# Optimization experiments

Hardware: AMD Instinct MI355X
Metric: run time of the kernel (lower is better)

The kernel has to match this reference:

```python
import jax, jax.numpy as jnp
import numpy as np

NEG_INF = -9e15
LEAKY_SLOPE = 0.01  # torch F.leaky_relu default


def setup_inputs() -> dict:
    key = jax.random.key(0)
    k1, k2, k3, k4 = jax.random.split(key, 4)
    N, F = 8192, 128
    inp = jax.random.normal(k1, (N, F), dtype=jnp.float32)
    adj = jax.random.randint(k2, (N, N), 0, 2, dtype=jnp.int32)
    # xavier_uniform with gain=1.414
    gain = 1.414
    limW = gain * np.sqrt(6.0 / (F + F))
    W = jax.random.uniform(k3, (F, F), minval=-limW, maxval=limW, dtype=jnp.float32)
    lima = gain * np.sqrt(6.0 / (2 * F + 1))
    a = jax.random.uniform(k4, (2 * F, 1), minval=-lima, maxval=lima, dtype=jnp.float32)
    return {"input": inp, "adj": adj, "W": W, "a": a}


def reference(input, adj, W, a):
    F_ = W.shape[0]
    h = input @ W                               # [N, F]
    # a_input[i,j] = concat(h[i], h[j]); (a_input @ a)[i,j] = h[i]@a1 + h[j]@a2
    a1, a2 = a[:F_, 0], a[F_:, 0]               # [F], [F]
    s1 = h @ a1                                 # [N]
    s2 = h @ a2                                 # [N]
    e = jax.nn.leaky_relu(s1[:, None] + s2[None, :], negative_slope=LEAKY_SLOPE)  # [N, N]
    masked = jnp.where(adj > 0, e, jnp.float32(NEG_INF))
    attention = jax.nn.softmax(masked, axis=1)  # [N, N]
    return attention @ h                        # [N, F]
```

## Files before the change

kernel.cpp:

```cpp
#include <hip/hip_runtime.h>
#include <hip/hip_bf16.h>

#define NN 8192
#define FF 128

typedef unsigned short ushort_t;
typedef __attribute__((ext_vector_type(4))) float f32x4;
typedef __attribute__((ext_vector_type(4))) int i32x4;
typedef __attribute__((ext_vector_type(8))) short s16x8;

__global__ __launch_bounds__(256)
void k1_hw(const float* __restrict__ inp, const float* __restrict__ W,
           const float* __restrict__ a, ushort_t* __restrict__ hT,
           float* __restrict__ s1g, float* __restrict__ Ug, float* __restrict__ Vg)
{
  __shared__ float Wl[FF * FF];
  __shared__ float il[32 * 129];
  __shared__ float red1[32 * 8];
  __shared__ float red2[32 * 8];
  const int t = threadIdx.x;
  const int ib = blockIdx.x * 32;

  {
    const float4* Ws = (const float4*)W;
    float4* Wd = (float4*)Wl;
#pragma unroll
    for (int q = 0; q < 16; ++q) Wd[t + 256 * q] = Ws[t + 256 * q];
  }
#pragma unroll
  for (int q = 0; q < 4; ++q) {
    int idx = t + 256 * q;
    int r = idx >> 5, c4 = idx & 31;
    float4 v = ((const float4*)(inp + (size_t)(ib + r) * FF))[c4];
    float* dst = &il[r * 129 + c4 * 4];
    dst[0] = v.x; dst[1] = v.y; dst[2] = v.z; dst[3] = v.w;
  }
  __syncthreads();

  const int r = t & 31;
  const int c0 = (t >> 5) * 16;
  float acc[16];
#pragma unroll
  for (int j = 0; j < 16; ++j) acc[j] = 0.f;

#pragma unroll 4
  for (int k = 0; k < FF; ++k) {
    float iv = il[r * 129 + k];
    const float4* wrow = (const float4*)&Wl[k * FF + c0];
    float4 w0 = wrow[0], w1 = wrow[1], w2 = wrow[2], w3 = wrow[3];
    acc[0]  += iv * w0.x; acc[1]  += iv * w0.y; acc[2]  += iv * w0.z; acc[3]  += iv * w0.w;
    acc[4]  += iv * w1.x; acc[5]  += iv * w1.y; acc[6]  += iv * w1.z; acc[7]  += iv * w1.w;
    acc[8]  += iv * w2.x; acc[9]  += iv * w2.y; acc[10] += iv * w2.z; acc[11] += iv * w2.w;
    acc[12] += iv * w3.x; acc[13] += iv * w3.y; acc[14] += iv * w3.z; acc[15] += iv * w3.w;
  }

  float ps1 = 0.f, ps2 = 0.f;
#pragma unroll
  for (int q = 0; q < 4; ++q) {
    float4 a1v = *(const float4*)(a + c0 + 4 * q);
    float4 a2v = *(const float4*)(a + FF + c0 + 4 * q);
    ps1 += acc[4*q+0]*a1v.x + acc[4*q+1]*a1v.y + acc[4*q+2]*a1v.z + acc[4*q+3]*a1v.w;
    ps2 += acc[4*q+0]*a2v.x + acc[4*q+1]*a2v.y + acc[4*q+2]*a2v.z + acc[4*q+3]*a2v.w;
  }
  red1[r * 8 + (t >> 5)] = ps1;
  red2[r * 8 + (t >> 5)] = ps2;

#pragma unroll
  for (int j = 0; j < 16; ++j) {
    unsigned b = __float_as_uint(acc[j]);
    hT[(unsigned)(c0 + j) * NN + (unsigned)(ib + r)] = (ushort_t)((b + 0x8000u) >> 16);
  }
  __syncthreads();
  if (t < 32) {
    float s1 = 0.f, s2 = 0.f;
#pragma unroll
    for (int g2 = 0; g2 < 8; ++g2) { s1 += red1[t * 8 + g2]; s2 += red2[t * 8 + g2]; }
    s1g[ib + t] = s1;
    Ug[ib + t] = expf(s2);
    Vg[ib + t] = expf(0.01f * s2);
  }
}

__global__ __launch_bounds__(512, 2)
void k3_attn(const int* __restrict__ adj, const float* __restrict__ s1g,
             const float* __restrict__ Ug, const float* __restrict__ Vg,
             const ushort_t* __restrict__ hT, float* __restrict__ out)
{
  __shared__ float accL[8][16][128];
  __shared__ float zL[8][16];

  const int t = threadIdx.x;
  const int lane = t & 63, w = t >> 6;
  const int rowl = lane & 15, kq = lane >> 4;
  const int rb = blockIdx.x * 16;
  const int jb = w * 1024 + kq * 8;

  const float s1v = s1g[rb + rowl];
  const float lv = s1v > 0.f ? s1v : 0.01f * s1v;
  const float P = expf(s1v - lv - 24.f);
  const float Q = expf(0.01f * s1v - lv - 24.f);
  const float E = expf(-s1v);

  f32x4 acc[8];
#pragma unroll
  for (int n = 0; n < 8; ++n) { acc[n][0] = 0.f; acc[n][1] = 0.f; acc[n][2] = 0.f; acc[n][3] = 0.f; }
  float z = 0.f;

  const i32x4* adjv = (const i32x4*)(adj + (size_t)(rb + rowl) * NN + jb);
  const float4* Uv = (const float4*)(Ug + jb);
  const float4* Vv = (const float4*)(Vg + jb);
  const ushort_t* hp[8];
#pragma unroll
  for (int n = 0; n < 8; ++n) hp[n] = hT + (size_t)(n * 16 + rowl) * NN + jb;

#pragma unroll 2
  for (int ks = 0; ks < 32; ++ks) {
    i32x4 A0 = __builtin_nontemporal_load(adjv + ks * 8);
    i32x4 A1 = __builtin_nontemporal_load(adjv + ks * 8 + 1);
    float4 u0 = Uv[ks * 8], u1 = Uv[ks * 8 + 1];
    float4 v0 = Vv[ks * 8], v1 = Vv[ks * 8 + 1];

    float w0 = u0.x > E ? P * u0.x : Q * v0.x;  w0 = A0[0] > 0 ? w0 : 0.f;
    float w1 = u0.y > E ? P * u0.y : Q * v0.y;  w1 = A0[1] > 0 ? w1 : 0.f;
    float w2 = u0.z > E ? P * u0.z : Q * v0.z;  w2 = A0[2] > 0 ? w2 : 0.f;
    float w3 = u0.w > E ? P * u0.w : Q * v0.w;  w3 = A0[3] > 0 ? w3 : 0.f;
    float w4 = u1.x > E ? P * u1.x : Q * v1.x;  w4 = A1[0] > 0 ? w4 : 0.f;
    float w5 = u1.y > E ? P * u1.y : Q * v1.y;  w5 = A1[1] > 0 ? w5 : 0.f;
    float w6 = u1.z > E ? P * u1.z : Q * v1.z;  w6 = A1[2] > 0 ? w6 : 0.f;
    float w7 = u1.w > E ? P * u1.w : Q * v1.w;  w7 = A1[3] > 0 ? w7 : 0.f;
    z += ((w0 + w1) + (w2 + w3)) + ((w4 + w5) + (w6 + w7));

    unsigned p0 = ((__float_as_uint(w0) + 0x8000u) >> 16) | ((__float_as_uint(w1) + 0x8000u) & 0xFFFF0000u);
    unsigned p1 = ((__float_as_uint(w2) + 0x8000u) >> 16) | ((__float_as_uint(w3) + 0x8000u) & 0xFFFF0000u);
    unsigned p2 = ((__float_as_uint(w4) + 0x8000u) >> 16) | ((__float_as_uint(w5) + 0x8000u) & 0xFFFF0000u);
    unsigned p3 = ((__float_as_uint(w6) + 0x8000u) >> 16) | ((__float_as_uint(w7) + 0x8000u) & 0xFFFF0000u);
    union { unsigned u[4]; s16x8 v; } afu;
    afu.u[0] = p0; afu.u[1] = p1; afu.u[2] = p2; afu.u[3] = p3;
    s16x8 af = afu.v;

#pragma unroll
    for (int n = 0; n < 8; ++n) {
      s16x8 bf = *(const s16x8*)(hp[n] + ks * 32);
      acc[n] = __builtin_amdgcn_mfma_f32_16x16x32_bf16(af, bf, acc[n], 0, 0, 0);
    }
  }

  z += __shfl_xor(z, 16);
  z += __shfl_xor(z, 32);

#pragma unroll
  for (int n = 0; n < 8; ++n)
#pragma unroll
    for (int r2 = 0; r2 < 4; ++r2)
      accL[w][kq * 4 + r2][n * 16 + rowl] = acc[n][r2];
  if (lane < 16) zL[w][lane] = z;
  __syncthreads();

  {
    const int idx = t * 4;
    const int row = idx >> 7, col = idx & 127;
    f32x4 s; s[0] = 0.f; s[1] = 0.f; s[2] = 0.f; s[3] = 0.f;
    float zs = 0.f;
#pragma unroll
    for (int w2 = 0; w2 < 8; ++w2) {
      s += *(const f32x4*)&accL[w2][row][col];
      zs += zL[w2][row];
    }
    const float rz = 1.f / zs;
    float4 o;
    o.x = s[0] * rz; o.y = s[1] * rz; o.z = s[2] * rz; o.w = s[3] * rz;
    *(float4*)(out + (size_t)(rb + row) * FF + col) = o;
  }
}

extern "C" void kernel_launch(void* const* d_in, const int* in_sizes, int n_in,
                              void* d_out, int out_size, void* d_ws, size_t ws_size,
                              hipStream_t stream)
{
  const float* inp = (const float*)d_in[0];
  const int* adj   = (const int*)d_in[1];
  const float* W   = (const float*)d_in[2];
  const float* a   = (const float*)d_in[3];
  float* out = (float*)d_out;

  char* ws = (char*)d_ws;
  ushort_t* hT = (ushort_t*)ws;
  float* s1g = (float*)(ws + (size_t)(2u << 20));
  float* Ug  = (float*)(ws + (size_t)(2u << 20) + (32u << 10));
  float* Vg  = (float*)(ws + (size_t)(2u << 20) + (64u << 10));

  hipLaunchKernelGGL(k1_hw, dim3(256), dim3(256), 0, stream, inp, W, a, hT, s1g, Ug, Vg);
  hipLaunchKernelGGL(k3_attn, dim3(512), dim3(512), 0, stream, adj, s1g, Ug, Vg, hT, out);
}
```

Before: 494.9 us.

## Coalesce adjacency loads row-wise and stage bf16 weights through swizzled LDS

```diff
diff --git a/kernel.cpp b/kernel.cpp
--- a/kernel.cpp
+++ b/kernel.cpp
@@ -81,19 +81,19 @@
   }
 }
 
-__global__ __launch_bounds__(512, 2)
+__global__ __launch_bounds__(512, 4)
 void k3_attn(const int* __restrict__ adj, const float* __restrict__ s1g,
              const float* __restrict__ Ug, const float* __restrict__ Vg,
              const ushort_t* __restrict__ hT, float* __restrict__ out)
 {
-  __shared__ float accL[8][16][128];
+  __shared__ __align__(16) char smem[65536];
   __shared__ float zL[8][16];
 
   const int t = threadIdx.x;
   const int lane = t & 63, w = t >> 6;
   const int rowl = lane & 15, kq = lane >> 4;
   const int rb = blockIdx.x * 16;
-  const int jb = w * 1024 + kq * 8;
+  const int jb0 = w * 1024;
 
   const float s1v = s1g[rb + rowl];
   const float lv = s1v > 0.f ? s1v : 0.01f * s1v;
@@ -101,59 +101,67 @@
   const float Q = expf(0.01f * s1v - lv - 24.f);
   const float E = expf(-s1v);
 
-  f32x4 acc[8];
+  f32x4 acc[8], acc9;
 #pragma unroll
   for (int n = 0; n < 8; ++n) { acc[n][0] = 0.f; acc[n][1] = 0.f; acc[n][2] = 0.f; acc[n][3] = 0.f; }
-  float z = 0.f;
-
-  const i32x4* adjv = (const i32x4*)(adj + (size_t)(rb + rowl) * NN + jb);
-  const float4* Uv = (const float4*)(Ug + jb);
-  const float4* Vv = (const float4*)(Vg + jb);
+  acc9[0] = 0.f; acc9[1] = 0.f; acc9[2] = 0.f; acc9[3] = 0.f;
+
+  char* wt = smem + w * 8192;
+
   const ushort_t* hp[8];
 #pragma unroll
-  for (int n = 0; n < 8; ++n) hp[n] = hT + (size_t)(n * 16 + rowl) * NN + jb;
-
-#pragma unroll 2
-  for (int ks = 0; ks < 32; ++ks) {
-    i32x4 A0 = __builtin_nontemporal_load(adjv + ks * 8);
-    i32x4 A1 = __builtin_nontemporal_load(adjv + ks * 8 + 1);
-    float4 u0 = Uv[ks * 8], u1 = Uv[ks * 8 + 1];
-    float4 v0 = Vv[ks * 8], v1 = Vv[ks * 8 + 1];
-
-    float w0 = u0.x > E ? P * u0.x : Q * v0.x;  w0 = A0[0] > 0 ? w0 : 0.f;
-    float w1 = u0.y > E ? P * u0.y : Q * v0.y;  w1 = A0[1] > 0 ? w1 : 0.f;
-    float w2 = u0.z > E ? P * u0.z : Q * v0.z;  w2 = A0[2] > 0 ? w2 : 0.f;
-    float w3 = u0.w > E ? P * u0.w : Q * v0.w;  w3 = A0[3] > 0 ? w3 : 0.f;
-    float w4 = u1.x > E ? P * u1.x : Q * v1.x;  w4 = A1[0] > 0 ? w4 : 0.f;
-    float w5 = u1.y > E ? P * u1.y : Q * v1.y;  w5 = A1[1] > 0 ? w5 : 0.f;
-    float w6 = u1.z > E ? P * u1.z : Q * v1.z;  w6 = A1[2] > 0 ? w6 : 0.f;
-    float w7 = u1.w > E ? P * u1.w : Q * v1.w;  w7 = A1[3] > 0 ? w7 : 0.f;
-    z += ((w0 + w1) + (w2 + w3)) + ((w4 + w5) + (w6 + w7));
-
-    unsigned p0 = ((__float_as_uint(w0) + 0x8000u) >> 16) | ((__float_as_uint(w1) + 0x8000u) & 0xFFFF0000u);
-    unsigned p1 = ((__float_as_uint(w2) + 0x8000u) >> 16) | ((__float_as_uint(w3) + 0x8000u) & 0xFFFF0000u);
-    unsigned p2 = ((__float_as_uint(w4) + 0x8000u) >> 16) | ((__float_as_uint(w5) + 0x8000u) & 0xFFFF0000u);
-    unsigned p3 = ((__float_as_uint(w6) + 0x8000u) >> 16) | ((__float_as_uint(w7) + 0x8000u) & 0xFFFF0000u);
-    union { unsigned u[4]; s16x8 v; } afu;
-    afu.u[0] = p0; afu.u[1] = p1; afu.u[2] = p2; afu.u[3] = p3;
-    s16x8 af = afu.v;
-
-#pragma unroll
-    for (int n = 0; n < 8; ++n) {
-      s16x8 bf = *(const s16x8*)(hp[n] + ks * 32);
-      acc[n] = __builtin_amdgcn_mfma_f32_16x16x32_bf16(af, bf, acc[n], 0, 0, 0);
+  for (int n = 0; n < 8; ++n) hp[n] = hT + (size_t)(n * 16 + rowl) * NN + jb0 + kq * 8;
+
+  union { unsigned u[4]; s16x8 v; } onesu;
+  onesu.u[0] = 0x3F803F80u; onesu.u[1] = 0x3F803F80u;
+  onesu.u[2] = 0x3F803F80u; onesu.u[3] = 0x3F803F80u;
+  const s16x8 ones = onesu.v;
+
+  const int wr_off = (((lane >> 1)) << 4) + ((lane & 1) << 3);
+  const int aoff = rowl * 512;
+
+  for (int sub = 0; sub < 4; ++sub) {
+    const int jbase = jb0 + sub * 256;
+    const float4 Uq = *(const float4*)(Ug + jbase + lane * 4);
+    const float4 Vq = *(const float4*)(Vg + jbase + lane * 4);
+
+#pragma unroll
+    for (int r = 0; r < 16; ++r) {
+      const i32x4 A = *((const i32x4*)(adj + (size_t)(rb + r) * NN + jbase) + lane);
+      const float Pr = __shfl(P, r);
+      const float Qr = __shfl(Q, r);
+      const float Er = __shfl(E, r);
+      float w0 = Uq.x > Er ? Pr * Uq.x : Qr * Vq.x;  w0 = A[0] > 0 ? w0 : 0.f;
+      float w1 = Uq.y > Er ? Pr * Uq.y : Qr * Vq.y;  w1 = A[1] > 0 ? w1 : 0.f;
+      float w2 = Uq.z > Er ? Pr * Uq.z : Qr * Vq.z;  w2 = A[2] > 0 ? w2 : 0.f;
+      float w3 = Uq.w > Er ? Pr * Uq.w : Qr * Vq.w;  w3 = A[3] > 0 ? w3 : 0.f;
+      unsigned p0 = ((__float_as_uint(w0) + 0x8000u) >> 16) | ((__float_as_uint(w1) + 0x8000u) & 0xFFFF0000u);
+      unsigned p1 = ((__float_as_uint(w2) + 0x8000u) >> 16) | ((__float_as_uint(w3) + 0x8000u) & 0xFFFF0000u);
+      *(uint2*)(wt + r * 512 + (wr_off ^ ((r & 7) << 4))) = make_uint2(p0, p1);
     }
-  }
-
-  z += __shfl_xor(z, 16);
-  z += __shfl_xor(z, 32);
-
+
+#pragma unroll
+    for (int kc = 0; kc < 8; ++kc) {
+      const s16x8 af = *(const s16x8*)(wt + aoff + (((kc * 4 + kq) ^ (rowl & 7)) << 4));
+#pragma unroll
+      for (int n = 0; n < 8; ++n) {
+        const s16x8 bf = *(const s16x8*)(hp[n] + sub * 256 + kc * 32);
+        acc[n] = __builtin_amdgcn_mfma_f32_16x16x32_bf16(af, bf, acc[n], 0, 0, 0);
+      }
+      acc9 = __builtin_amdgcn_mfma_f32_16x16x32_bf16(af, ones, acc9, 0, 0, 0);
+    }
+  }
+
+  if (rowl == 0) {
+#pragma unroll
+    for (int r2 = 0; r2 < 4; ++r2) zL[w][kq * 4 + r2] = acc9[r2];
+  }
+  float* accW = (float*)(smem + w * 8192);
 #pragma unroll
   for (int n = 0; n < 8; ++n)
 #pragma unroll
     for (int r2 = 0; r2 < 4; ++r2)
-      accL[w][kq * 4 + r2][n * 16 + rowl] = acc[n][r2];
-  if (lane < 16) zL[w][lane] = z;
+      accW[(kq * 4 + r2) * 128 + n * 16 + rowl] = acc[n][r2];
   __syncthreads();
 
   {
@@ -163,7 +171,7 @@
     float zs = 0.f;
 #pragma unroll
     for (int w2 = 0; w2 < 8; ++w2) {
-      s += *(const f32x4*)&accL[w2][row][col];
+      s += *(const f32x4*)(smem + w2 * 8192 + ((row * 128 + col) << 2));
       zs += zL[w2][row];
     }
     const float rz = 1.f / zs;
```

Measured after the change: 519.8 us. +5.0%, slower.
